# Optimization experiments

Measured on AMD Instinct MI355X. Metric: run time of the kernel, lower is better.

The kernel has to match this reference:

```python
import jax, jax.numpy as jnp
import numpy as np

B, C, H, W = 4, 256, 64, 64
CQK = C // 8

def setup_inputs() -> dict:
    key = jax.random.key(0)
    ks = jax.random.split(key, 8)
    s = 0.02
    return {
        "x": jax.random.normal(ks[0], (B, C, H, W), dtype=jnp.float32),
        "wq": jax.random.normal(ks[1], (CQK, C), dtype=jnp.float32) * s,
        "bq": jnp.zeros((CQK,), dtype=jnp.float32),
        "wk": jax.random.normal(ks[2], (CQK, C), dtype=jnp.float32) * s,
        "bk": jnp.zeros((CQK,), dtype=jnp.float32),
        "wv": jax.random.normal(ks[3], (C, C), dtype=jnp.float32) * s,
        "bv": jnp.zeros((C,), dtype=jnp.float32),
        "gamma": jnp.zeros((1,), dtype=jnp.float32),
    }

def reference(x, wq, bq, wk, bk, wv, bv, gamma):
    b, c, h, w = x.shape
    n = h * w
    xf = x.reshape(b, c, n)                                  # [B,C,N]
    q = jnp.einsum('oc,bcn->bon', wq, xf) + bq[None, :, None]  # [B,CQK,N]
    k = jnp.einsum('oc,bcn->bon', wk, xf) + bk[None, :, None]  # [B,CQK,N]
    v = jnp.einsum('oc,bcn->bon', wv, xf) + bv[None, :, None]  # [B,C,N]
    energy = jnp.einsum('bdi,bdj->bij', q, k)                # [B,N,N]  Q^T K
    attn = jax.nn.softmax(energy, axis=-1)
    out = jnp.einsum('bcj,bij->bci', v, attn)                # V @ attn^T
    out = out.reshape(b, c, h, w)
    return gamma * out + x
```

## Files before the change

kernel.cpp:

```cpp
#include <hip/hip_runtime.h>
#include <math.h>

static const int Bn   = 4;
static const int Cn   = 256;
static const int Dqk  = 32;
static const int Nn   = 4096;
static const int TI   = 32;
static const int NBLK_ATT = Bn * (Nn / TI);

__global__ __launch_bounds__(256) void qkv_kernel(
    const float* __restrict__ x,
    const float* __restrict__ wq, const float* __restrict__ bq,
    const float* __restrict__ wk, const float* __restrict__ bk,
    const float* __restrict__ wv, const float* __restrict__ bv,
    const float* __restrict__ gamma,
    float* __restrict__ ws)
{
    if (gamma[0] == 0.0f) return;

    const int blk = blockIdx.x;
    const int b   = blk / (Nn / TI);
    const int i0  = (blk % (Nn / TI)) * TI;

    __shared__ float xs[Cn][TI];
    const float* xb = x + (size_t)b * Cn * Nn;
    for (int idx = threadIdx.x; idx < Cn * TI; idx += 256) {
        int c = idx / TI, i = idx % TI;
        xs[c][i] = xb[(size_t)c * Nn + i0 + i];
    }
    __syncthreads();

    float* qw = ws;
    float* kw = ws + (size_t)Bn * Dqk * Nn;
    float* vw = kw + (size_t)Bn * Dqk * Nn;

    for (int idx = threadIdx.x; idx < (2 * Dqk + Cn) * TI; idx += 256) {
        int r = idx / TI, i = idx % TI;
        const float* wrow; float bias; float* dst;
        if (r < Dqk) {
            wrow = wq + (size_t)r * Cn; bias = bq[r];
            dst  = qw + ((size_t)b * Dqk + r) * Nn;
        } else if (r < 2 * Dqk) {
            int rr = r - Dqk;
            wrow = wk + (size_t)rr * Cn; bias = bk[rr];
            dst  = kw + ((size_t)b * Dqk + rr) * Nn;
        } else {
            int rr = r - 2 * Dqk;
            wrow = wv + (size_t)rr * Cn; bias = bv[rr];
            dst  = vw + ((size_t)b * Cn + rr) * Nn;
        }
        float acc = bias;
        for (int c = 0; c < Cn; ++c) acc += wrow[c] * xs[c][i];
        dst[i0 + i] = acc;
    }
}

__global__ __launch_bounds__(256) void attn_out_kernel(
    const float* __restrict__ x,
    const float* __restrict__ gamma,
    const float* __restrict__ ws,
    int has_ws,
    float* __restrict__ out)
{
    const float g = gamma[0];
    const int t = threadIdx.x;

    if (g == 0.0f || !has_ws) {
        size_t gid = (size_t)blockIdx.x * 256 + t;
        const float4* src = (const float4*)x;
        float4* dst = (float4*)out;
        dst[gid] = src[gid];
        return;
    }

    const int blk = blockIdx.x;
    if (blk >= NBLK_ATT) return;
    const int b  = blk / (Nn / TI);
    const int i0 = (blk % (Nn / TI)) * TI;

    const float* qw = ws;
    const float* kw = ws + (size_t)Bn * Dqk * Nn;
    const float* vw = kw + (size_t)Bn * Dqk * Nn;
    const float* xb = x   + (size_t)b * Cn * Nn;
    float*       ob = out + (size_t)b * Cn * Nn;

    __shared__ float qs[Dqk][TI];
    __shared__ float ks[Dqk][TI];
    __shared__ float ps[TI][TI];
    __shared__ float vs[Cn][TI];
    __shared__ float m_s[TI], l_s[TI], alpha_s[TI];

    for (int idx = t; idx < Dqk * TI; idx += 256) {
        int d = idx / TI, ii = idx % TI;
        qs[d][ii] = qw[((size_t)b * Dqk + d) * Nn + i0 + ii];
    }
    if (t < TI) { m_s[t] = -1e30f; l_s[t] = 0.0f; }

    const int ii = t & 31;
    const int c0 = (t >> 5) * 32;
    float acc[32];
#pragma unroll
    for (int cc = 0; cc < 32; ++cc) acc[cc] = 0.0f;
    __syncthreads();

    for (int j0 = 0; j0 < Nn; j0 += TI) {
        for (int idx = t; idx < Dqk * TI; idx += 256) {
            int d = idx / TI, jj = idx % TI;
            ks[d][jj] = kw[((size_t)b * Dqk + d) * Nn + j0 + jj];
        }
        for (int idx = t; idx < Cn * TI; idx += 256) {
            int c = idx / TI, jj = idx % TI;
            vs[c][jj] = vw[((size_t)b * Cn + c) * Nn + j0 + jj];
        }
        __syncthreads();

        for (int idx = t; idx < TI * TI; idx += 256) {
            int i2 = idx / TI, j2 = idx % TI;
            float e = 0.0f;
            for (int d = 0; d < Dqk; ++d) e += qs[d][i2] * ks[d][j2];
            ps[i2][j2] = e;
        }
        __syncthreads();

        if (t < TI) {
            float mold = m_s[t], mnew = mold;
            for (int j2 = 0; j2 < TI; ++j2) mnew = fmaxf(mnew, ps[t][j2]);
            float al = __expf(mold - mnew);
            float lsum = 0.0f;
            for (int j2 = 0; j2 < TI; ++j2) {
                float p = __expf(ps[t][j2] - mnew);
                ps[t][j2] = p;
                lsum += p;
            }
            m_s[t] = mnew;
            l_s[t] = l_s[t] * al + lsum;
            alpha_s[t] = al;
        }
        __syncthreads();

        const float al = alpha_s[ii];
#pragma unroll
        for (int cc = 0; cc < 32; ++cc) acc[cc] *= al;
        for (int j2 = 0; j2 < TI; ++j2) {
            float p = ps[ii][j2];
#pragma unroll
            for (int cc = 0; cc < 32; ++cc) acc[cc] += p * vs[c0 + cc][j2];
        }
        __syncthreads();
    }

    const float linv = 1.0f / l_s[ii];
    for (int cc = 0; cc < 32; ++cc) {
        size_t off = (size_t)(c0 + cc) * Nn + i0 + ii;
        ob[off] = xb[off] + g * acc[cc] * linv;
    }
}

extern "C" void kernel_launch(void* const* d_in, const int* in_sizes, int n_in,
                              void* d_out, int out_size, void* d_ws, size_t ws_size,
                              hipStream_t stream) {
    (void)in_sizes; (void)n_in; (void)out_size;
    const float* x     = (const float*)d_in[0];
    const float* wq    = (const float*)d_in[1];
    const float* bq    = (const float*)d_in[2];
    const float* wk    = (const float*)d_in[3];
    const float* bk    = (const float*)d_in[4];
    const float* wv    = (const float*)d_in[5];
    const float* bv    = (const float*)d_in[6];
    const float* gamma = (const float*)d_in[7];
    float* out = (float*)d_out;
    float* ws  = (float*)d_ws;

    const size_t ws_needed = (size_t)(2 * Dqk + Cn) * Bn * Nn * sizeof(float);
    const int has_ws = ws_size >= ws_needed;

    if (has_ws) {
        qkv_kernel<<<NBLK_ATT, 256, 0, stream>>>(x, wq, bq, wk, bk, wv, bv, gamma, ws);
    }
    attn_out_kernel<<<4096, 256, 0, stream>>>(x, gamma, ws, has_ws, out);
}
```

Before: 82.12 us.

## Fuse QKV projection into attention kernel and drop the separate launch

Merges the QKV projection into the attention kernel, recomputing K and V from x for each key tile instead of staging them in workspace, so there is a single launch. The gamma==0 copy path now uses 1024 blocks, each moving four float4s per thread. Since gamma is zero in the test inputs, what matters is removing the second launch (qkv_kernel, which returned early) and the larger copy grid. When gamma is nonzero the fused path recomputes the projections for every query block, a large amount of redundant arithmetic.

```diff
diff --git a/kernel.cpp b/kernel.cpp
--- a/kernel.cpp
+++ b/kernel.cpp
@@ -8,68 +8,33 @@
 static const int TI   = 32;
 static const int NBLK_ATT = Bn * (Nn / TI);
 
-__global__ __launch_bounds__(256) void qkv_kernel(
+static const int NBLK  = 1024;
+static const int NF4   = Bn * Cn * Nn / 4;
+static const int STRIDE = NBLK * 256;
+
+__global__ __launch_bounds__(256) void selfattn2d_kernel(
     const float* __restrict__ x,
     const float* __restrict__ wq, const float* __restrict__ bq,
     const float* __restrict__ wk, const float* __restrict__ bk,
     const float* __restrict__ wv, const float* __restrict__ bv,
     const float* __restrict__ gamma,
-    float* __restrict__ ws)
-{
-    if (gamma[0] == 0.0f) return;
-
-    const int blk = blockIdx.x;
-    const int b   = blk / (Nn / TI);
-    const int i0  = (blk % (Nn / TI)) * TI;
-
-    __shared__ float xs[Cn][TI];
-    const float* xb = x + (size_t)b * Cn * Nn;
-    for (int idx = threadIdx.x; idx < Cn * TI; idx += 256) {
-        int c = idx / TI, i = idx % TI;
-        xs[c][i] = xb[(size_t)c * Nn + i0 + i];
-    }
-    __syncthreads();
-
-    float* qw = ws;
-    float* kw = ws + (size_t)Bn * Dqk * Nn;
-    float* vw = kw + (size_t)Bn * Dqk * Nn;
-
-    for (int idx = threadIdx.x; idx < (2 * Dqk + Cn) * TI; idx += 256) {
-        int r = idx / TI, i = idx % TI;
-        const float* wrow; float bias; float* dst;
-        if (r < Dqk) {
-            wrow = wq + (size_t)r * Cn; bias = bq[r];
-            dst  = qw + ((size_t)b * Dqk + r) * Nn;
-        } else if (r < 2 * Dqk) {
-            int rr = r - Dqk;
-            wrow = wk + (size_t)rr * Cn; bias = bk[rr];
-            dst  = kw + ((size_t)b * Dqk + rr) * Nn;
-        } else {
-            int rr = r - 2 * Dqk;
-            wrow = wv + (size_t)rr * Cn; bias = bv[rr];
-            dst  = vw + ((size_t)b * Cn + rr) * Nn;
-        }
-        float acc = bias;
-        for (int c = 0; c < Cn; ++c) acc += wrow[c] * xs[c][i];
-        dst[i0 + i] = acc;
-    }
-}
-
-__global__ __launch_bounds__(256) void attn_out_kernel(
-    const float* __restrict__ x,
-    const float* __restrict__ gamma,
-    const float* __restrict__ ws,
-    int has_ws,
     float* __restrict__ out)
 {
     const float g = gamma[0];
     const int t = threadIdx.x;
 
-    if (g == 0.0f || !has_ws) {
+    if (g == 0.0f) {
+        const float4* __restrict__ src = (const float4*)x;
+        float4* __restrict__ dst = (float4*)out;
         size_t gid = (size_t)blockIdx.x * 256 + t;
-        const float4* src = (const float4*)x;
-        float4* dst = (float4*)out;
-        dst[gid] = src[gid];
+        float4 r0 = src[gid];
+        float4 r1 = src[gid + STRIDE];
+        float4 r2 = src[gid + 2 * (size_t)STRIDE];
+        float4 r3 = src[gid + 3 * (size_t)STRIDE];
+        dst[gid]                      = r0;
+        dst[gid + STRIDE]             = r1;
+        dst[gid + 2 * (size_t)STRIDE] = r2;
+        dst[gid + 3 * (size_t)STRIDE] = r3;
         return;
     }
 
@@ -78,21 +43,27 @@
     const int b  = blk / (Nn / TI);
     const int i0 = (blk % (Nn / TI)) * TI;
 
-    const float* qw = ws;
-    const float* kw = ws + (size_t)Bn * Dqk * Nn;
-    const float* vw = kw + (size_t)Bn * Dqk * Nn;
     const float* xb = x   + (size_t)b * Cn * Nn;
     float*       ob = out + (size_t)b * Cn * Nn;
 
+    __shared__ float xs[Cn][TI];
     __shared__ float qs[Dqk][TI];
     __shared__ float ks[Dqk][TI];
     __shared__ float ps[TI][TI];
-    __shared__ float vs[Cn][TI];
+    __shared__ float vchunk[64][TI];
     __shared__ float m_s[TI], l_s[TI], alpha_s[TI];
 
+    for (int idx = t; idx < Cn * TI; idx += 256) {
+        int c = idx / TI, i = idx % TI;
+        xs[c][i] = xb[(size_t)c * Nn + i0 + i];
+    }
+    __syncthreads();
     for (int idx = t; idx < Dqk * TI; idx += 256) {
-        int d = idx / TI, ii = idx % TI;
-        qs[d][ii] = qw[((size_t)b * Dqk + d) * Nn + i0 + ii];
+        int r = idx / TI, i = idx % TI;
+        float acc = bq[r];
+        const float* wrow = wq + (size_t)r * Cn;
+        for (int c = 0; c < Cn; ++c) acc += wrow[c] * xs[c][i];
+        qs[r][i] = acc;
     }
     if (t < TI) { m_s[t] = -1e30f; l_s[t] = 0.0f; }
 
@@ -104,16 +75,19 @@
     __syncthreads();
 
     for (int j0 = 0; j0 < Nn; j0 += TI) {
-        for (int idx = t; idx < Dqk * TI; idx += 256) {
-            int d = idx / TI, jj = idx % TI;
-            ks[d][jj] = kw[((size_t)b * Dqk + d) * Nn + j0 + jj];
-        }
         for (int idx = t; idx < Cn * TI; idx += 256) {
             int c = idx / TI, jj = idx % TI;
-            vs[c][jj] = vw[((size_t)b * Cn + c) * Nn + j0 + jj];
+            xs[c][jj] = xb[(size_t)c * Nn + j0 + jj];
         }
         __syncthreads();
-
+        for (int idx = t; idx < Dqk * TI; idx += 256) {
+            int r = idx / TI, jj = idx % TI;
+            float a = bk[r];
+            const float* wrow = wk + (size_t)r * Cn;
+            for (int c = 0; c < Cn; ++c) a += wrow[c] * xs[c][jj];
+            ks[r][jj] = a;
+        }
+        __syncthreads();
         for (int idx = t; idx < TI * TI; idx += 256) {
             int i2 = idx / TI, j2 = idx % TI;
             float e = 0.0f;
@@ -121,7 +95,6 @@
             ps[i2][j2] = e;
         }
         __syncthreads();
-
         if (t < TI) {
             float mold = m_s[t], mnew = mold;
             for (int j2 = 0; j2 < TI; ++j2) mnew = fmaxf(mnew, ps[t][j2]);
@@ -141,12 +114,27 @@
         const float al = alpha_s[ii];
 #pragma unroll
         for (int cc = 0; cc < 32; ++cc) acc[cc] *= al;
-        for (int j2 = 0; j2 < TI; ++j2) {
-            float p = ps[ii][j2];
+
+        for (int cb = 0; cb < Cn; cb += 64) {
+            for (int idx = t; idx < 64 * TI; idx += 256) {
+                int r = idx / TI, jj = idx % TI;
+                float a = bv[cb + r];
+                const float* wrow = wv + (size_t)(cb + r) * Cn;
+                for (int c = 0; c < Cn; ++c) a += wrow[c] * xs[c][jj];
+                vchunk[r][jj] = a;
+            }
+            __syncthreads();
+            if (c0 >= cb && c0 < cb + 64) {
+                const int roff = c0 - cb;
+                for (int j2 = 0; j2 < TI; ++j2) {
+                    float p = ps[ii][j2];
 #pragma unroll
-            for (int cc = 0; cc < 32; ++cc) acc[cc] += p * vs[c0 + cc][j2];
+                    for (int cc = 0; cc < 32; ++cc)
+                        acc[cc] += p * vchunk[roff + cc][j2];
+                }
+            }
+            __syncthreads();
         }
-        __syncthreads();
     }
 
     const float linv = 1.0f / l_s[ii];
@@ -159,7 +147,7 @@
 extern "C" void kernel_launch(void* const* d_in, const int* in_sizes, int n_in,
                               void* d_out, int out_size, void* d_ws, size_t ws_size,
                               hipStream_t stream) {
-    (void)in_sizes; (void)n_in; (void)out_size;
+    (void)in_sizes; (void)n_in; (void)out_size; (void)d_ws; (void)ws_size;
     const float* x     = (const float*)d_in[0];
     const float* wq    = (const float*)d_in[1];
     const float* bq    = (const float*)d_in[2];
@@ -169,13 +157,6 @@
     const float* bv    = (const float*)d_in[6];
     const float* gamma = (const float*)d_in[7];
     float* out = (float*)d_out;
-    float* ws  = (float*)d_ws;
 
-    const size_t ws_needed = (size_t)(2 * Dqk + Cn) * Bn * Nn * sizeof(float);
-    const int has_ws = ws_size >= ws_needed;
-
-    if (has_ws) {
-        qkv_kernel<<<NBLK_ATT, 256, 0, stream>>>(x, wq, bq, wk, bk, wv, bv, gamma, ws);
-    }
-    attn_out_kernel<<<4096, 256, 0, stream>>>(x, gamma, ws, has_ws, out);
+    selfattn2d_kernel<<<NBLK, 256, 0, stream>>>(x, wq, bq, wk, bk, wv, bv, gamma, out);
 }
```

Result: no change. 80.76 us (-1.7%).
